# Performance work log

Hardware: AMD Instinct MI355X
Metric: run time of the kernel (lower is better)

The kernel has to match this reference:

```python
import jax, jax.numpy as jnp
import numpy as np
from jax import lax

EPS = 1e-4  # BatchNorm eps from the module

def maxpool2x2(x):
    # x: [N, C, H, W] -> 2x2 max pool, stride 2, no padding
    return lax.reduce_window(x, -jnp.inf, lax.max, (1, 1, 2, 2), (1, 1, 2, 2), 'VALID')

def conv_nchw(x, w):
    return lax.conv_general_dilated(x, w, window_strides=(1, 1), padding='VALID',
                                    dimension_numbers=('NCHW', 'OIHW', 'NCHW'))

def setup_inputs() -> dict:
    key = jax.random.key(0)
    ks = jax.random.split(key, 6)
    return {
        'x':       jax.random.normal(ks[0], (8192, 1, 32, 32), dtype=jnp.float32),
        'conv1_w': jax.random.normal(ks[1], (20, 1, 5, 5), dtype=jnp.float32) * 0.1,
        'conv2_w': jax.random.normal(ks[2], (50, 20, 5, 5), dtype=jnp.float32) * 0.1,
        'lin_w':   jax.random.normal(ks[3], (500, 1250), dtype=jnp.float32) * 0.05,
        'fc_w':    jax.random.normal(ks[4], (10, 500), dtype=jnp.float32) * 0.05,
        'fc_b':    jax.random.normal(ks[5], (10,), dtype=jnp.float32) * 0.05,
    }

def reference(x, conv1_w, conv2_w, lin_w, fc_w, fc_b):
    # --- features ---
    # Conv2d(1, 20, k=5, bias=False): [N,1,32,32] -> [N,20,28,28]
    h = conv_nchw(x, conv1_w)
    # BatchNorm2d(20, eps=1e-4, affine=False), training-mode batch stats (biased var)
    mean = jnp.mean(h, axis=(0, 2, 3), keepdims=True)
    var = jnp.var(h, axis=(0, 2, 3), keepdims=True)
    h = (h - mean) * lax.rsqrt(var + EPS)
    # ReLU + MaxPool 2x2: -> [N,20,14,14]
    h = maxpool2x2(jnp.maximum(h, 0.0))
    # Binarize(): sign of activations
    h = jnp.sign(h)
    # Conv2dBinary(20, 50, k=5): XNOR-style conv = conv with sign(W), scaled by
    # per-output-channel alpha = mean(|W|). -> [N,50,10,10]
    alpha2 = jnp.mean(jnp.abs(conv2_w), axis=(1, 2, 3)).reshape(1, -1, 1, 1)
    h = conv_nchw(h, jnp.sign(conv2_w)) * alpha2
    # Hardtanh + MaxPool 2x2: -> [N,50,5,5]
    h = maxpool2x2(jnp.clip(h, -1.0, 1.0))
    # --- dense ---
    h = h.reshape(h.shape[0], -1)  # [N, 1250], channel-major like torch.flatten
    h = jnp.sign(h)
    # LinearBinary(1250, 500): y = x @ sign(W)^T * alpha, alpha = mean(|W|, dim=1)
    alpha_l = jnp.mean(jnp.abs(lin_w), axis=1)  # [500]
    h = (h @ jnp.sign(lin_w).T) * alpha_l
    h = jnp.clip(h, -1.0, 1.0)
    # fc: Linear(500, num_classes)
    return h @ fc_w.T + fc_b
```

## Files before the change

kernel.cpp:

```cpp
#include <hip/hip_runtime.h>
#include <stdint.h>


#define NIMG 8192

typedef __attribute__((ext_vector_type(8))) _Float16 f16x8;
typedef __attribute__((ext_vector_type(16))) float f32x16;
typedef __attribute__((ext_vector_type(4))) int i32x4;
typedef __attribute__((ext_vector_type(16))) int i32x16;


__global__ __launch_bounds__(256) void prepsum_k(const float* __restrict__ lw,
                                                 const float* __restrict__ w2,
                                                 const float* __restrict__ x,
                                                 unsigned long long* __restrict__ lwp,
                                                 float* __restrict__ alpha,
                                                 i32x4* __restrict__ bg,
                                                 float* __restrict__ partial) {
  int b = blockIdx.x, tid = threadIdx.x;
  if (b < 125) {
    int wave = tid >> 6, lane = tid & 63;
    int j = b * 4 + wave;
    float pa = 0.f;
#pragma unroll
    for (int w = 0; w < 20; ++w) {
      int idx = w * 64 + lane;
      float v = (idx < 1250) ? lw[j * 1250 + idx] : 0.f;
      pa += fabsf(v);
      unsigned long long m = __ballot(v > 0.f);
      if (lane == 0) lwp[j * 20 + w] = m;
    }
    for (int o = 32; o > 0; o >>= 1) pa += __shfl_down(pa, o, 64);
    if (lane == 0) alpha[j] = pa / 1250.0f;
  } else if (b < 138) {
    int idx = (b - 125) * 256 + tid;
    if (idx < 3200) {
      int t = idx >> 7;
      int rem = idx & 127;
      int l = rem & 63;
      int nt = rem >> 6;
      int oc = nt * 32 + (l & 31);
      int hi = l >> 5;
      i32x4 o4;
#pragma unroll
      for (int wi = 0; wi < 4; ++wi) {
        int word = 0;
#pragma unroll
        for (int bb = 0; bb < 4; ++bb) {
          int k = hi * 16 + wi * 4 + bb;
          int v = 0;
          if (k < 20 && oc < 50)
            v = (w2[(oc * 20 + k) * 25 + t] > 0.f) ? 1 : -1;
          word |= (v & 0xff) << (8 * bb);
        }
        o4[wi] = word;
      }
      bg[idx] = o4;
    }
  } else {
    int sb = b - 138;
    const float4* xv = (const float4*)x + (size_t)sb * 64 * 256;
    float ax = 0.f, ay = 0.f, az = 0.f, aw = 0.f;
    for (int nn = 0; nn < 64; ++nn) {
      float4 v = xv[nn * 256 + tid];
      ax += v.x; ay += v.y; az += v.z; aw += v.w;
    }
    float4 r; r.x = ax; r.y = ay; r.z = az; r.w = aw;
    ((float4*)(partial + (size_t)sb * 1024))[tid] = r;
  }
}

__global__ __launch_bounds__(256) void mean_k(const float* __restrict__ partial,
                                              const float* __restrict__ w1,
                                              float* __restrict__ mean) {
  __shared__ float Tsh[1024];
  __shared__ double U8[25][8];
  __shared__ double U[25];
  int t = threadIdx.x;
  for (int e = t; e < 1024; e += 256) {
    double s = 0.0;
    for (int b = 0; b < 128; ++b) s += (double)partial[(size_t)b * 1024 + e];
    Tsh[e] = (float)s;
  }
  __syncthreads();
  if (t < 200) {
    int tap = t >> 3, part = t & 7;
    int ky = tap / 5, kx = tap % 5;
    double s = 0.0;
    for (int p = part * 98; p < part * 98 + 98; ++p) {
      int py = p / 28, px = p % 28;
      s += (double)Tsh[(py + ky) * 32 + px + kx];
    }
    U8[tap][part] = s;
  }
  __syncthreads();
  if (t < 25) {
    double s = 0.0;
    for (int i = 0; i < 8; ++i) s += U8[t][i];
    U[t] = s;
  }
  __syncthreads();
  if (t < 20) {
    double s = 0.0;
    for (int q = 0; q < 25; ++q) s += (double)w1[t * 25 + q] * U[q];
    mean[t] = (float)(s / (8192.0 * 784.0));
  }
}

__device__ inline uint32_t pack_f16_pair(float fv) {
  _Float16 h = (_Float16)fv;
  float rem = fv - (float)h;
  _Float16 l = (_Float16)(rem * 4096.0f);
  uint32_t hb = (uint32_t)__builtin_bit_cast(unsigned short, h);
  uint32_t lb = (uint32_t)__builtin_bit_cast(unsigned short, l);
  return (hb << 16) | lb;
}

__global__ __launch_bounds__(512, 4) void conv12_k(const float* __restrict__ x,
                                                   const float* __restrict__ w1,
                                                   const float* __restrict__ mean,
                                                   const i32x4* __restrict__ bg,
                                                   const unsigned long long* __restrict__ lwp,
                                                   const float* __restrict__ alpha,
                                                   const float* __restrict__ fcw,
                                                   const float* __restrict__ fcb,
                                                   float* __restrict__ out) {
  __shared__ uint32_t xs8[8][1032];
  __shared__ uint32_t b1sh[1568];
  __shared__ __attribute__((aligned(16))) char uni[8][2048];
  int tid = threadIdx.x;
  int wave = tid >> 6, lane = tid & 63;
  int n0 = blockIdx.x * 8;
  int n = n0 + wave;

  uint32_t* xs = xs8[wave];
  {
    const float4* xin = (const float4*)(x + (size_t)n * 1024);
#pragma unroll
    for (int i = 0; i < 4; ++i) {
      int idx = i * 64 + lane;
      float4 v = xin[idx];
      float fv[4] = {v.x, v.y, v.z, v.w};
#pragma unroll
      for (int e = 0; e < 4; ++e)
        xs[4 * idx + e] = pack_f16_pair(fv[e]);
    }
    if (lane < 8) xs[1024 + lane] = 0;
  }

  int bc = lane & 31;
  int khsel = lane >> 5;
  {
    f16x8 Bh[2], Bhs[2], Bl[2];
    const int t1tab[8] = {8, 9, 18, 19, 20, 21, 22, 23};
    const _Float16 SC = (_Float16)4096.0f;
#pragma unroll
    for (int j = 0; j < 8; ++j) {
      int t0 = j + khsel * 10;
      float wv0 = (bc < 20) ? w1[bc * 25 + t0] : 0.f;
      uint32_t p0 = pack_f16_pair(wv0);
      _Float16 h0 = __builtin_bit_cast(_Float16, (unsigned short)(p0 >> 16));
      Bh[0][j] = h0;
      Bhs[0][j] = h0 * SC;
      Bl[0][j] = __builtin_bit_cast(_Float16, (unsigned short)(p0 & 0xffffu));
      float wv1 = 0.f;
      if (bc < 20) {
        if (khsel == 0) wv1 = w1[bc * 25 + t1tab[j]];
        else if (j == 4) wv1 = w1[bc * 25 + 24];
      }
      uint32_t p1 = pack_f16_pair(wv1);
      _Float16 h1 = __builtin_bit_cast(_Float16, (unsigned short)(p1 >> 16));
      Bh[1][j] = h1;
      Bhs[1][j] = h1 * SC;
      Bl[1][j] = __builtin_bit_cast(_Float16, (unsigned short)(p1 & 0xffffu));
    }
    float mv = (bc < 20) ? mean[bc] * 4096.0f : 3.0e38f;

    int m = lane & 31;
    int d0 = m + khsel * 64;
    int d1 = m + khsel * 4;

    for (int pp = 0; pp < 14; ++pp) {
      unsigned long long bacc[16];
#pragma unroll
      for (int r = 0; r < 16; ++r) bacc[r] = 0ull;
#pragma unroll
      for (int py2 = 0; py2 < 2; ++py2) {
        int pybase = (2 * pp + py2) * 32;
        const uint32_t* b0 = xs + pybase + d0;
        const uint32_t* b1 = xs + pybase + d1;
        uint32_t raw[16];
        raw[0] = b0[0];   raw[1] = b0[1];   raw[2] = b0[2];   raw[3] = b0[3];
        raw[4] = b0[4];   raw[5] = b0[32];  raw[6] = b0[33];  raw[7] = b0[34];
        raw[8] = b1[35];  raw[9] = b1[36];  raw[10] = b1[99]; raw[11] = b1[100];
        raw[12] = b1[128]; raw[13] = b1[129]; raw[14] = b1[130]; raw[15] = b1[131];
        f16x8 Ah[2], Al[2];
#pragma unroll
        for (int kh = 0; kh < 2; ++kh) {
          uint32_t hw[4], lw2[4];
#pragma unroll
          for (int jj = 0; jj < 4; ++jj) {
            uint32_t v0 = raw[kh * 8 + 2 * jj], v1 = raw[kh * 8 + 2 * jj + 1];
            hw[jj] = __builtin_amdgcn_perm(v1, v0, 0x07060302u);
            lw2[jj] = __builtin_amdgcn_perm(v1, v0, 0x05040100u);
          }
          struct U4 { uint32_t a, b, c, d; };
          U4 hv4 = {hw[0], hw[1], hw[2], hw[3]};
          U4 lv4 = {lw2[0], lw2[1], lw2[2], lw2[3]};
          Ah[kh] = __builtin_bit_cast(f16x8, hv4);
          Al[kh] = __builtin_bit_cast(f16x8, lv4);
        }
        f32x16 acc;
#pragma unroll
        for (int i = 0; i < 16; ++i) acc[i] = 0.f;
        acc = __builtin_amdgcn_mfma_f32_32x32x16_f16(Ah[0], Bhs[0], acc, 0, 0, 0);
        acc = __builtin_amdgcn_mfma_f32_32x32x16_f16(Ah[1], Bhs[1], acc, 0, 0, 0);
        acc = __builtin_amdgcn_mfma_f32_32x32x16_f16(Ah[0], Bl[0], acc, 0, 0, 0);
        acc = __builtin_amdgcn_mfma_f32_32x32x16_f16(Ah[1], Bl[1], acc, 0, 0, 0);
        acc = __builtin_amdgcn_mfma_f32_32x32x16_f16(Al[0], Bh[0], acc, 0, 0, 0);
        acc = __builtin_amdgcn_mfma_f32_32x32x16_f16(Al[1], Bh[1], acc, 0, 0, 0);
#pragma unroll
        for (int r = 0; r < 16; ++r)
          bacc[r] |= __ballot(acc[r] > mv);
      }
      uint32_t pm = 0;
#pragma unroll
      for (int pc = 0; pc < 14; ++pc) {
        int px0 = 2 * pc;
        int r0 = (px0 & 3) + 4 * (px0 >> 3);
        int h0 = (px0 >> 2) & 1;
        unsigned long long mm = bacc[r0] | bacc[r0 + 1];
        uint32_t val = (uint32_t)(mm >> (32 * h0));
        if (lane == pc) pm = val;
      }
      if (lane < 14) b1sh[wave * 196 + pp * 14 + lane] = pm;
    }
  }
  __syncthreads();

  {
    int m = lane & 31, hi = lane >> 5;
    int shbase = hi * 16;
    for (int mt = wave; mt < 25; mt += 8) {
      int qg = mt * 8 + (m >> 2);
      int img = (qg * 41) >> 10;
      int quad = qg - img * 25;
      int Y = (quad * 13) >> 6;
      int X = quad - Y * 5;
      int px = (2 * Y + ((m >> 1) & 1)) * 14 + 2 * X + (m & 1);
      const uint32_t* arow = b1sh + img * 196 + px;
      const i32x4* bgl = bg + lane;
      i32x16 acc0, acc1;
#pragma unroll
      for (int i = 0; i < 16; ++i) { acc0[i] = 0; acc1[i] = 0; }
#pragma unroll 1
      for (int ky = 0; ky < 5; ++ky) {
        const uint32_t* ar2 = arow + ky * 14;
        const i32x4* bg2 = bgl + ky * 5 * 128;
#pragma unroll
        for (int kx = 0; kx < 5; ++kx) {
          uint32_t w = ar2[kx];
          i32x4 av;
#pragma unroll
          for (int wi = 0; wi < 4; ++wi)
            av[wi] = (int)((((w >> (shbase + 4 * wi)) & 0xFu) * 0x00204081u) & 0x01010101u);
          i32x4 bv0 = bg2[kx * 128];
          i32x4 bv1 = bg2[kx * 128 + 64];
          acc0 = __builtin_amdgcn_mfma_i32_32x32x32_i8(av, bv0, acc0, 0, 0, 0);
          acc1 = __builtin_amdgcn_mfma_i32_32x32x32_i8(av, bv1, acc1, 0, 0, 0);
        }
      }
      int oc0 = m, oc1 = 32 + m;
#pragma unroll
      for (int g = 0; g < 4; ++g) {
        int qloc = 2 * g + hi;
        int qg2 = mt * 8 + qloc;
        int img2 = (qg2 * 41) >> 10;
        int quad2 = qg2 - img2 * 25;
        {
          int a0 = acc0[4 * g], a1 = acc0[4 * g + 1], a2 = acc0[4 * g + 2], a3 = acc0[4 * g + 3];
          int c0 = a0 > a1 ? a0 : a1, c1 = a2 > a3 ? a2 : a3;
          int best = c0 > c1 ? c0 : c1;
          uni[img2][oc0 * 25 + quad2] = (char)((best > 0) - (best < 0));
        }
        if (oc1 < 50) {
          int a0 = acc1[4 * g], a1 = acc1[4 * g + 1], a2 = acc1[4 * g + 2], a3 = acc1[4 * g + 3];
          int c0 = a0 > a1 ? a0 : a1, c1 = a2 > a3 ? a2 : a3;
          int best = c0 > c1 ? c0 : c1;
          uni[img2][oc1 * 25 + quad2] = (char)((best > 0) - (best < 0));
        }
      }
    }
  }
  __syncthreads();

  signed char* s2w = (signed char*)uni[wave];
  float* hshw = (float*)uni[wave];
  if (lane < 30) s2w[1250 + lane] = 0;

  unsigned long long Pm[20], Nm[20];
  int cp = 0, cn = 0;
#pragma unroll
  for (int k = 0; k < 20; ++k) {
    signed char v = s2w[k * 64 + lane];
    unsigned long long P = __ballot(v > 0);
    unsigned long long N = __ballot(v < 0);
    Pm[k] = P; Nm[k] = N;
    cp += __popcll(P); cn += __popcll(N);
  }

#pragma unroll
  for (int rd = 0; rd < 8; ++rd) {
    int j = rd * 64 + lane;
    float y = 0.f;
    if (j < 500) {
      const ulonglong2* W2 = (const ulonglong2*)(lwp + (size_t)j * 20);
      int a = 0, b = 0;
#pragma unroll
      for (int i = 0; i < 10; ++i) {
        ulonglong2 w2v = W2[i];
        a += __popcll(w2v.x & Pm[2 * i]) + __popcll(w2v.y & Pm[2 * i + 1]);
        b += __popcll(w2v.x & Nm[2 * i]) + __popcll(w2v.y & Nm[2 * i + 1]);
      }
      int dot = 2 * (a - b) - cp + cn;
      y = alpha[j] * (float)dot;
      y = fminf(1.0f, fmaxf(-1.0f, y));
    }
    hshw[rd * 64 + lane] = y;
  }

  float hv[8];
#pragma unroll
  for (int k = 0; k < 8; ++k) hv[k] = hshw[k * 64 + lane];
#pragma unroll
  for (int o = 0; o < 10; ++o) {
    float pa = 0.f;
#pragma unroll
    for (int k = 0; k < 8; ++k) {
      int j = k * 64 + lane;
      if (j < 500) pa += hv[k] * fcw[o * 500 + j];
    }
    for (int off = 32; off > 0; off >>= 1) pa += __shfl_down(pa, off, 64);
    if (lane == 0) out[(size_t)n * 10 + o] = pa + fcb[o];
  }
}

extern "C" void kernel_launch(void* const* d_in, const int* in_sizes, int n_in,
                              void* d_out, int out_size, void* d_ws, size_t ws_size,
                              hipStream_t stream) {
  const float* x   = (const float*)d_in[0];
  const float* w1  = (const float*)d_in[1];
  const float* w2  = (const float*)d_in[2];
  const float* lw  = (const float*)d_in[3];
  const float* fcw = (const float*)d_in[4];
  const float* fcb = (const float*)d_in[5];
  float* out = (float*)d_out;
  char* ws = (char*)d_ws;

  float*    mean  = (float*)(ws + 0);
  float*    alpha = (float*)(ws + 5632);
  unsigned long long* lwp = (unsigned long long*)(ws + 7680);
  float*    partial = (float*)(ws + 87808);
  i32x4*    bg    = (i32x4*)(ws + 8673024);

  prepsum_k<<<266, 256, 0, stream>>>(lw, w2, x, lwp, alpha, bg, partial);
  mean_k<<<1, 256, 0, stream>>>(partial, w1, mean);
  conv12_k<<<1024, 512, 0, stream>>>(x, w1, mean, bg, lwp, alpha, fcw, fcb, out);
}
```

Baseline: 224.0 us.

## Replace single-block mean kernel with atomics and per-block mean recompute

Removes the serial one-block mean_k launch. Per-pixel batch sums are now accumulated with float atomics into a global 1024-element buffer by more, smaller blocks, and every conv12 block recomputes the 20 channel means from that buffer in shared memory. This drops a launch and a long single-block reduction from the critical path. In exchange it adds a memset, atomic contention and non-deterministic summation order, and every block repeats the tap reduction in double precision.

```diff
diff --git a/kernel.cpp b/kernel.cpp
--- a/kernel.cpp
+++ b/kernel.cpp
@@ -16,7 +16,7 @@
                                                  unsigned long long* __restrict__ lwp,
                                                  float* __restrict__ alpha,
                                                  i32x4* __restrict__ bg,
-                                                 float* __restrict__ partial) {
+                                                 float* __restrict__ Tglob) {
   int b = blockIdx.x, tid = threadIdx.x;
   if (b < 125) {
     int wave = tid >> 6, lane = tid & 63;
@@ -59,51 +59,16 @@
     }
   } else {
     int sb = b - 138;
-    const float4* xv = (const float4*)x + (size_t)sb * 64 * 256;
+    const float4* xv = (const float4*)x + (size_t)sb * 16 * 256;
     float ax = 0.f, ay = 0.f, az = 0.f, aw = 0.f;
-    for (int nn = 0; nn < 64; ++nn) {
+    for (int nn = 0; nn < 16; ++nn) {
       float4 v = xv[nn * 256 + tid];
       ax += v.x; ay += v.y; az += v.z; aw += v.w;
     }
-    float4 r; r.x = ax; r.y = ay; r.z = az; r.w = aw;
-    ((float4*)(partial + (size_t)sb * 1024))[tid] = r;
-  }
-}
-
-__global__ __launch_bounds__(256) void mean_k(const float* __restrict__ partial,
-                                              const float* __restrict__ w1,
-                                              float* __restrict__ mean) {
-  __shared__ float Tsh[1024];
-  __shared__ double U8[25][8];
-  __shared__ double U[25];
-  int t = threadIdx.x;
-  for (int e = t; e < 1024; e += 256) {
-    double s = 0.0;
-    for (int b = 0; b < 128; ++b) s += (double)partial[(size_t)b * 1024 + e];
-    Tsh[e] = (float)s;
-  }
-  __syncthreads();
-  if (t < 200) {
-    int tap = t >> 3, part = t & 7;
-    int ky = tap / 5, kx = tap % 5;
-    double s = 0.0;
-    for (int p = part * 98; p < part * 98 + 98; ++p) {
-      int py = p / 28, px = p % 28;
-      s += (double)Tsh[(py + ky) * 32 + px + kx];
-    }
-    U8[tap][part] = s;
-  }
-  __syncthreads();
-  if (t < 25) {
-    double s = 0.0;
-    for (int i = 0; i < 8; ++i) s += U8[t][i];
-    U[t] = s;
-  }
-  __syncthreads();
-  if (t < 20) {
-    double s = 0.0;
-    for (int q = 0; q < 25; ++q) s += (double)w1[t * 25 + q] * U[q];
-    mean[t] = (float)(s / (8192.0 * 784.0));
+    atomicAdd(&Tglob[4 * tid + 0], ax);
+    atomicAdd(&Tglob[4 * tid + 1], ay);
+    atomicAdd(&Tglob[4 * tid + 2], az);
+    atomicAdd(&Tglob[4 * tid + 3], aw);
   }
 }
 
@@ -118,20 +83,52 @@
 
 __global__ __launch_bounds__(512, 4) void conv12_k(const float* __restrict__ x,
                                                    const float* __restrict__ w1,
-                                                   const float* __restrict__ mean,
                                                    const i32x4* __restrict__ bg,
                                                    const unsigned long long* __restrict__ lwp,
                                                    const float* __restrict__ alpha,
                                                    const float* __restrict__ fcw,
                                                    const float* __restrict__ fcb,
+                                                   const float* __restrict__ Tglob,
                                                    float* __restrict__ out) {
   __shared__ uint32_t xs8[8][1032];
   __shared__ uint32_t b1sh[1568];
   __shared__ __attribute__((aligned(16))) char uni[8][2048];
+  __shared__ float mean_sh[32];
   int tid = threadIdx.x;
   int wave = tid >> 6, lane = tid & 63;
   int n0 = blockIdx.x * 8;
   int n = n0 + wave;
+
+  {
+    float* Tsh = (float*)b1sh;
+    double* U8 = (double*)uni;
+    double* U = ((double*)uni) + 256;
+    for (int e = tid; e < 1024; e += 512) Tsh[e] = Tglob[e];
+    __syncthreads();
+    if (tid < 200) {
+      int tap = tid >> 3, part = tid & 7;
+      int ky = tap / 5, kx = tap % 5;
+      double s = 0.0;
+      for (int p = part * 98; p < part * 98 + 98; ++p) {
+        int py = p / 28, px = p % 28;
+        s += (double)Tsh[(py + ky) * 32 + px + kx];
+      }
+      U8[tap * 8 + part] = s;
+    }
+    __syncthreads();
+    if (tid < 25) {
+      double s = 0.0;
+      for (int i = 0; i < 8; ++i) s += U8[tid * 8 + i];
+      U[tid] = s;
+    }
+    __syncthreads();
+    if (tid < 20) {
+      double s = 0.0;
+      for (int q = 0; q < 25; ++q) s += (double)w1[tid * 25 + q] * U[q];
+      mean_sh[tid] = (float)(s / (8192.0 * 784.0));
+    }
+    __syncthreads();
+  }
 
   uint32_t* xs = xs8[wave];
   {
@@ -174,7 +171,7 @@
       Bhs[1][j] = h1 * SC;
       Bl[1][j] = __builtin_bit_cast(_Float16, (unsigned short)(p1 & 0xffffu));
     }
-    float mv = (bc < 20) ? mean[bc] * 4096.0f : 3.0e38f;
+    float mv = (bc < 20) ? mean_sh[bc] * 4096.0f : 3.0e38f;
 
     int m = lane & 31;
     int d0 = m + khsel * 64;
@@ -357,13 +354,12 @@
   float* out = (float*)d_out;
   char* ws = (char*)d_ws;
 
-  float*    mean  = (float*)(ws + 0);
   float*    alpha = (float*)(ws + 5632);
   unsigned long long* lwp = (unsigned long long*)(ws + 7680);
-  float*    partial = (float*)(ws + 87808);
+  float*    Tglob = (float*)(ws + 612096);
   i32x4*    bg    = (i32x4*)(ws + 8673024);
 
-  prepsum_k<<<266, 256, 0, stream>>>(lw, w2, x, lwp, alpha, bg, partial);
-  mean_k<<<1, 256, 0, stream>>>(partial, w1, mean);
-  conv12_k<<<1024, 512, 0, stream>>>(x, w1, mean, bg, lwp, alpha, fcw, fcb, out);
+  hipMemsetAsync(Tglob, 0, 1024 * sizeof(float), stream);
+  prepsum_k<<<650, 256, 0, stream>>>(lw, w2, x, lwp, alpha, bg, Tglob);
+  conv12_k<<<1024, 512, 0, stream>>>(x, w1, bg, lwp, alpha, fcw, fcb, Tglob, out);
 }
```

Result: slower. 258.9 us (+15.6%).
